# Kernel tuning notes

Measured on AMD Instinct MI355X. Metric: run time of the kernel, lower is better.

The kernel has to match this reference:

```python
import jax, jax.numpy as jnp
import numpy as np

B, S, H, D, R = 2, 2048, 16, 128, 16
HID = H * D
ROPE_BASE = 10000.0


def _rotate_half(x):
    x1, x2 = x[..., : D // 2], x[..., D // 2:]
    return jnp.concatenate((-x2, x1), axis=-1)


def _sin_cos(position_ids):
    # full-dim RoPE (rope_fraction == 1)
    inv_freq = 1.0 / (ROPE_BASE ** (jnp.arange(0, D, 2, dtype=jnp.float32) / D))  # [D/2]
    freqs = position_ids.astype(jnp.float32)[..., None] * inv_freq  # [B,S,D/2]
    emb = jnp.concatenate((freqs, freqs), axis=-1)  # [B,S,D]
    # add head axis -> [B,1,S,D]
    return jnp.sin(emb)[:, None], jnp.cos(emb)[:, None]


def setup_inputs() -> dict:
    key = jax.random.key(0)
    ks = jax.random.split(key, 6)
    q = jax.random.normal(ks[0], (B, S, HID), dtype=jnp.float32)
    k = jax.random.normal(ks[1], (B, S, HID), dtype=jnp.float32)
    v = jax.random.normal(ks[2], (B, S, HID), dtype=jnp.float32)
    position_ids = jnp.tile(jnp.arange(S, dtype=jnp.int64)[None], (B, 1))
    causal = jnp.tril(jnp.ones((S, S), dtype=bool))
    attention_mask = jnp.where(causal, 0.0, -1e9).astype(jnp.float32)
    attention_mask = jnp.broadcast_to(attention_mask[None, None], (B, 1, S, S))
    k_registers = jax.random.normal(ks[3], (1, H, R, D), dtype=jnp.float32)
    v_registers = jax.random.normal(ks[4], (1, H, R, D), dtype=jnp.float32)
    return {
        "query_states": q,
        "key_states": k,
        "value_states": v,
        "position_ids": position_ids,
        "attention_mask": attention_mask,
        "k_registers": k_registers,
        "v_registers": v_registers,
    }


def reference(query_states, key_states, value_states, position_ids,
              attention_mask, k_registers, v_registers):
    bsz, q_len, _ = query_states.shape
    # [B,S,H*D] -> [B,H,S,D]
    q = query_states.reshape(bsz, q_len, H, D).transpose(0, 2, 1, 3)
    k = key_states.reshape(bsz, -1, H, D).transpose(0, 2, 1, 3)
    v = value_states.reshape(bsz, -1, H, D).transpose(0, 2, 1, 3)

    sin, cos = _sin_cos(position_ids)
    q = q * cos + _rotate_half(q) * sin
    k = k * cos + _rotate_half(k) * sin

    # concat learned register K/V tokens along kv-length
    k = jnp.concatenate((k, jnp.broadcast_to(k_registers, (bsz, H, R, D))), axis=2)
    v = jnp.concatenate((v, jnp.broadcast_to(v_registers, (bsz, H, R, D))), axis=2)
    mask = jnp.concatenate(
        (attention_mask,
         jnp.zeros(attention_mask.shape[:-1] + (R,), dtype=attention_mask.dtype)),
        axis=-1)

    scale = 1.0 / np.sqrt(D).astype(np.float32)
    scores = jnp.einsum('bhqd,bhkd->bhqk', q, k * scale) + mask  # [B,H,S,S+R]
    probs = jax.nn.softmax(scores.astype(jnp.float32), axis=-1).astype(q.dtype)
    out = jnp.einsum('bhqk,bhkd->bhqd', probs, v)
    return out.transpose(0, 2, 1, 3).reshape(bsz, q_len, H * D)
```

## Files before the change

### kernel.cpp

```cpp
#include <hip/hip_runtime.h>

#define S_LEN 2048
#define HID   2048
#define NH    16
#define HD    128
#define NREG  16
#define KPAD  2112
#define NBH   32

typedef float f32x4 __attribute__((ext_vector_type(4)));
typedef short s16x8 __attribute__((ext_vector_type(8)));

#define ROPE_C  0.20762050593046014f
#define INV2PI  0.15915494309189535f
#define TWOPI   6.283185307179586f
#define QSCALE  0.08838834764831845f

__device__ __forceinline__ unsigned short f2bf(float f) {
    union { float f; unsigned int u; } x; x.f = f;
    return (unsigned short)((x.u + 0x7FFFu + ((x.u >> 16) & 1u)) >> 16);
}
__device__ __forceinline__ unsigned short f2bf_t(float f) {
    union { float f; unsigned int u; } x; x.f = f;
    return (unsigned short)(x.u >> 16);
}
__device__ __forceinline__ void gl_lds16(const unsigned short* g, unsigned short* l) {
    __builtin_amdgcn_global_load_lds((const __attribute__((address_space(1))) void*)g,
                                     (__attribute__((address_space(3))) void*)l, 16, 0, 0);
}

__global__ void prep_kernel(const float* __restrict__ k, const float* __restrict__ v,
                            const int* __restrict__ pos,
                            const float* __restrict__ kreg, const float* __restrict__ vreg,
                            unsigned short* __restrict__ Kb, unsigned short* __restrict__ Vt) {
    int kt = blockIdx.x % 33;
    int bh = blockIdx.x / 33;
    int b = bh >> 4, h = bh & 15;
    int tid = threadIdx.x;

    {
        int dh = tid & 63, wv = tid >> 6;
        if (kt < 32) {
            float inv = exp2f((float)dh * -ROPE_C);
            #pragma unroll 4
            for (int j = 0; j < 16; ++j) {
                int key = wv * 16 + j;
                int s = kt * 64 + key;
                float p = (float)pos[b * S_LEN + s];
                float rev = p * inv * INV2PI;
                rev -= rintf(rev);
                float a2 = rev * TWOPI;
                float sn = __sinf(a2), cs = __cosf(a2);
                const float* kp = k + (size_t)(b * S_LEN + s) * HID + h * HD + dh;
                float k1 = kp[0], k2 = kp[64];
                size_t ko = (size_t)(bh * KPAD + s) * HD + dh;
                Kb[ko]      = f2bf(k1 * cs - k2 * sn);
                Kb[ko + 64] = f2bf(k2 * cs + k1 * sn);
            }
        } else {
            #pragma unroll 4
            for (int j = 0; j < 16; ++j) {
                int r = wv * 16 + j;
                float k1 = 0.f, k2 = 0.f;
                if (r < NREG) {
                    const float* kp = kreg + (h * NREG + r) * HD + dh;
                    k1 = kp[0]; k2 = kp[64];
                }
                size_t ko = (size_t)(bh * KPAD + 2048 + r) * HD + dh;
                Kb[ko]      = f2bf(k1);
                Kb[ko + 64] = f2bf(k2);
            }
        }
    }

    __shared__ unsigned short T[64][136];
    {
        int key = tid >> 2, c = tid & 3;
        #pragma unroll
        for (int i = 0; i < 4; ++i) {
            int d0 = c * 32 + i * 8;
            float vals[8];
            if (kt < 32) {
                const float* src = v + (size_t)(b * S_LEN + kt * 64 + key) * HID + h * HD + d0;
                float4 a = *(const float4*)src, bb = *(const float4*)(src + 4);
                vals[0]=a.x; vals[1]=a.y; vals[2]=a.z; vals[3]=a.w;
                vals[4]=bb.x; vals[5]=bb.y; vals[6]=bb.z; vals[7]=bb.w;
            } else if (key < NREG) {
                const float* src = vreg + (h * NREG + key) * HD + d0;
                float4 a = *(const float4*)src, bb = *(const float4*)(src + 4);
                vals[0]=a.x; vals[1]=a.y; vals[2]=a.z; vals[3]=a.w;
                vals[4]=bb.x; vals[5]=bb.y; vals[6]=bb.z; vals[7]=bb.w;
            } else {
                #pragma unroll
                for (int n = 0; n < 8; ++n) vals[n] = 0.f;
            }
            unsigned short tmp[8];
            #pragma unroll
            for (int n = 0; n < 8; ++n) tmp[n] = f2bf(vals[n]);
            *(uint4*)(&T[key][d0]) = *(const uint4*)tmp;
        }
    }
    __syncthreads();
    {
        int d = tid >> 1, half = tid & 1;
        unsigned short buf[32];
        #pragma unroll
        for (int i = 0; i < 32; ++i) buf[i] = T[half * 32 + i][d];
        uint4* dst = (uint4*)(Vt + ((size_t)(bh * HD + d)) * KPAD + kt * 64 + half * 32);
        const uint4* bp = (const uint4*)buf;
        #pragma unroll
        for (int i = 0; i < 4; ++i) dst[i] = bp[i];
    }
}

__global__ __launch_bounds__(256, 2)
void attn_kernel(const float* __restrict__ q, const int* __restrict__ pos,
                 const unsigned short* __restrict__ Kb, const unsigned short* __restrict__ Vt,
                 float* __restrict__ out) {
    __shared__ unsigned short Klds[64 * 128];
    __shared__ unsigned short Vtl[128 * 64];
    __shared__ unsigned short Plds[4 * 32 * 72];

    int idx = blockIdx.x;
    int bh  = idx & 31;
    int j5  = idx >> 5;
    int t   = (idx < 256) ? (15 - 2 * j5) : (2 * (j5 - 8));
    int b = bh >> 4, h = bh & 15;
    int tid = threadIdx.x, w = tid >> 6, lane = tid & 63;
    int quad = lane >> 4, k15 = lane & 15;
    int s0q = t * 128;

    const unsigned short* kg[4]; unsigned short* klp[4];
    const unsigned short* vg[4]; unsigned short* vlp[4];
    {
        int krow = 16 * w + (lane >> 4);
        #pragma unroll
        for (int j = 0; j < 4; ++j) {
            int key = krow + 4 * j;
            kg[j]  = Kb + ((size_t)bh * KPAD + key) * HD + (((lane & 15) ^ (key & 15)) << 3);
            klp[j] = Klds + (16 * w + 4 * j) * HD;
        }
        int drow = 32 * w + (lane >> 3);
        int vsw  = ((lane & 7) ^ (lane >> 3)) << 3;
        #pragma unroll
        for (int j = 0; j < 4; ++j) {
            vg[j]  = Vt + ((size_t)bh * HD + drow + 8 * j) * KPAD + vsw;
            vlp[j] = Vtl + (32 * w + 8 * j) * 64;
        }
    }

    s16x8 qa[2][4];
    #pragma unroll
    for (int mt = 0; mt < 2; ++mt) {
        int s = s0q + w * 32 + mt * 16 + k15;
        float pp = (float)pos[b * S_LEN + s];
        const float* qrow = q + (size_t)(b * S_LEN + s) * HID + h * HD + quad * 8;
        float lo[2][8], hi[2][8];
        #pragma unroll
        for (int kc = 0; kc < 2; ++kc) {
            float4 a  = *(const float4*)(qrow + kc * 32);
            float4 c  = *(const float4*)(qrow + kc * 32 + 4);
            lo[kc][0]=a.x; lo[kc][1]=a.y; lo[kc][2]=a.z; lo[kc][3]=a.w;
            lo[kc][4]=c.x; lo[kc][5]=c.y; lo[kc][6]=c.z; lo[kc][7]=c.w;
            float4 a2 = *(const float4*)(qrow + kc * 32 + 64);
            float4 c2 = *(const float4*)(qrow + kc * 32 + 68);
            hi[kc][0]=a2.x; hi[kc][1]=a2.y; hi[kc][2]=a2.z; hi[kc][3]=a2.w;
            hi[kc][4]=c2.x; hi[kc][5]=c2.y; hi[kc][6]=c2.z; hi[kc][7]=c2.w;
        }
        #pragma unroll
        for (int kc = 0; kc < 2; ++kc)
            #pragma unroll
            for (int j = 0; j < 8; ++j) {
                int dh = kc * 32 + quad * 8 + j;
                float inv = exp2f((float)dh * -ROPE_C);
                float rev = pp * inv * INV2PI;
                rev -= rintf(rev);
                float a2r = rev * TWOPI;
                float sn = __sinf(a2r), cs = __cosf(a2r);
                float qlo = lo[kc][j], qhi = hi[kc][j];
                qa[mt][kc][j]     = (short)f2bf((qlo * cs - qhi * sn) * QSCALE);
                qa[mt][kc + 2][j] = (short)f2bf((qhi * cs + qlo * sn) * QSCALE);
            }
    }

    f32x4 oacc[2][8];
    float lsum[2][4];
    #pragma unroll
    for (int mt = 0; mt < 2; ++mt) {
        #pragma unroll
        for (int nc = 0; nc < 8; ++nc) oacc[mt][nc] = (f32x4){0.f, 0.f, 0.f, 0.f};
        #pragma unroll
        for (int r = 0; r < 4; ++r) lsum[mt][r] = 0.f;
    }

    auto stage = [&](int kbase) {
        size_t ko = (size_t)kbase * HD;
        #pragma unroll
        for (int j = 0; j < 4; ++j) gl_lds16(kg[j] + ko, klp[j]);
        #pragma unroll
        for (int j = 0; j < 4; ++j) gl_lds16(vg[j] + kbase, vlp[j]);
    };

    auto tile = [&](int coff, int mode) {
        f32x4 sc[2][4];
        #pragma unroll
        for (int mt = 0; mt < 2; ++mt)
            #pragma unroll
            for (int nc = 0; nc < 4; ++nc) sc[mt][nc] = (f32x4){0.f, 0.f, 0.f, 0.f};
        #pragma unroll
        for (int kc = 0; kc < 4; ++kc)
            #pragma unroll
            for (int nc = 0; nc < 4; ++nc) {
                if (mode == 2 && nc > 0) continue;
                const s16x8 bf = *(const s16x8*)(Klds + (nc * 16 + k15) * HD +
                                                 (((4 * kc + quad) ^ k15) << 3));
                #pragma unroll
                for (int mt = 0; mt < 2; ++mt)
                    sc[mt][nc] = __builtin_amdgcn_mfma_f32_16x16x32_bf16(qa[mt][kc], bf, sc[mt][nc], 0, 0, 0);
            }
        #pragma unroll
        for (int mt = 0; mt < 2; ++mt) {
            int rowb = w * 32 + mt * 16 + quad * 4;
            #pragma unroll
            for (int r = 0; r < 4; ++r) {
                float p[4];
                #pragma unroll
                for (int nc = 0; nc < 4; ++nc) {
                    if (mode == 2 && nc > 0) { p[nc] = 0.f; continue; }
                    float e = __expf(sc[mt][nc][r]);
                    bool valid = (mode == 1) ? (coff + nc * 16 + k15 <= rowb + r)
                               : (mode == 2) ? (k15 < NREG) : true;
                    p[nc] = valid ? e : 0.f;
                }
                lsum[mt][r] += (p[0] + p[1]) + (p[2] + p[3]);
                int prow = w * (32 * 72) + (mt * 16 + quad * 4 + r) * 72 + k15;
                Plds[prow]      = f2bf_t(p[0]);
                Plds[prow + 16] = f2bf_t(p[1]);
                Plds[prow + 32] = f2bf_t(p[2]);
                Plds[prow + 48] = f2bf_t(p[3]);
            }
        }
        #pragma unroll
        for (int kc = 0; kc < 2; ++kc) {
            if (mode == 2 && kc > 0) break;
            s16x8 pf[2];
            #pragma unroll
            for (int mt = 0; mt < 2; ++mt)
                pf[mt] = *(const s16x8*)(Plds + w * (32 * 72) + (mt * 16 + k15) * 72 +
                                         kc * 32 + quad * 8);
            #pragma unroll
            for (int nc = 0; nc < 8; ++nc) {
                const s16x8 vf = *(const s16x8*)(Vtl + (nc * 16 + k15) * 64 +
                                                 (((4 * kc + quad) ^ (k15 & 7)) << 3));
                #pragma unroll
                for (int mt = 0; mt < 2; ++mt)
                    oacc[mt][nc] = __builtin_amdgcn_mfma_f32_16x16x32_bf16(pf[mt], vf, oacc[mt][nc], 0, 0, 0);
            }
        }
    };

    int nfull = 2 * t;
    for (int kt = 0; kt < nfull; ++kt) {
        __syncthreads();
        stage(kt * 64);
        __syncthreads();
        tile(0, 0);
    }
    #pragma unroll
    for (int dt = 0; dt < 2; ++dt) {
        __syncthreads();
        stage((2 * t + dt) * 64);
        __syncthreads();
        tile(64 * dt, 1);
    }
    __syncthreads();
    stage(2048);
    __syncthreads();
    tile(0, 2);

    #pragma unroll
    for (int mt = 0; mt < 2; ++mt)
        #pragma unroll
        for (int r = 0; r < 4; ++r) {
            float lv = lsum[mt][r];
            #pragma unroll
            for (int off = 1; off < 16; off <<= 1) lv += __shfl_xor(lv, off);
            float invl = 1.0f / lv;
            size_t row = (size_t)(b * S_LEN + s0q + w * 32 + mt * 16 + quad * 4 + r) * HID
                         + h * HD + k15;
            #pragma unroll
            for (int nc = 0; nc < 8; ++nc)
                out[row + nc * 16] = oacc[mt][nc][r] * invl;
        }
}

extern "C" void kernel_launch(void* const* d_in, const int* in_sizes, int n_in,
                              void* d_out, int out_size, void* d_ws, size_t ws_size,
                              hipStream_t stream) {
    const float* q    = (const float*)d_in[0];
    const float* k    = (const float*)d_in[1];
    const float* v    = (const float*)d_in[2];
    const int*   pos  = (const int*)d_in[3];
    const float* kreg = (const float*)d_in[5];
    const float* vreg = (const float*)d_in[6];
    float* out = (float*)d_out;

    unsigned short* Kb = (unsigned short*)d_ws;
    unsigned short* Vt = Kb + (size_t)NBH * KPAD * HD;

    prep_kernel<<<dim3(NBH * 33), dim3(256), 0, stream>>>(k, v, pos, kreg, vreg, Kb, Vt);
    attn_kernel<<<dim3(512), dim3(256), 0, stream>>>(q, pos, Kb, Vt, out);
}
```

Baseline: 226.9 us.

## Use 8 waves per block with double-buffered K staging

The attention kernel now runs 512 threads per block, so each wave owns 16 query rows instead of 32, which cuts per-wave register use (one m-tile instead of two). K tiles are double-buffered in LDS and the next K tile is prefetched while the current one is processed. V is still single-buffered and is staged alongside the K prefetch. The main loop is restructured with a barrier between score and PV phases. The trade-off is a higher wave count per block and the LDS cost of a second K buffer, with less MFMA reuse of each K/V fragment per wave.

```diff
diff --git a/kernel.cpp b/kernel.cpp
--- a/kernel.cpp
+++ b/kernel.cpp
@@ -113,13 +113,13 @@
     }
 }
 
-__global__ __launch_bounds__(256, 2)
+__global__ __launch_bounds__(512, 4)
 void attn_kernel(const float* __restrict__ q, const int* __restrict__ pos,
                  const unsigned short* __restrict__ Kb, const unsigned short* __restrict__ Vt,
                  float* __restrict__ out) {
-    __shared__ unsigned short Klds[64 * 128];
+    __shared__ unsigned short Klds[2][64 * 128];
     __shared__ unsigned short Vtl[128 * 64];
-    __shared__ unsigned short Plds[4 * 32 * 72];
+    __shared__ unsigned short Plds[8 * 16 * 72];
 
     int idx = blockIdx.x;
     int bh  = idx & 31;
@@ -130,29 +130,37 @@
     int quad = lane >> 4, k15 = lane & 15;
     int s0q = t * 128;
 
-    const unsigned short* kg[4]; unsigned short* klp[4];
-    const unsigned short* vg[4]; unsigned short* vlp[4];
-    {
-        int krow = 16 * w + (lane >> 4);
-        #pragma unroll
-        for (int j = 0; j < 4; ++j) {
-            int key = krow + 4 * j;
-            kg[j]  = Kb + ((size_t)bh * KPAD + key) * HD + (((lane & 15) ^ (key & 15)) << 3);
-            klp[j] = Klds + (16 * w + 4 * j) * HD;
-        }
-        int drow = 32 * w + (lane >> 3);
-        int vsw  = ((lane & 7) ^ (lane >> 3)) << 3;
-        #pragma unroll
-        for (int j = 0; j < 4; ++j) {
-            vg[j]  = Vt + ((size_t)bh * HD + drow + 8 * j) * KPAD + vsw;
-            vlp[j] = Vtl + (32 * w + 8 * j) * 64;
-        }
-    }
-
-    s16x8 qa[2][4];
-    #pragma unroll
-    for (int mt = 0; mt < 2; ++mt) {
-        int s = s0q + w * 32 + mt * 16 + k15;
+    const unsigned short* Kb_bh = Kb + (size_t)bh * KPAD * HD;
+    const unsigned short* Vt_bh = Vt + (size_t)bh * HD * KPAD;
+    int koff[2], klo[2], voff[2], vlo[2];
+    #pragma unroll
+    for (int j = 0; j < 2; ++j) {
+        int row = 4 * (w + 8 * j) + (lane >> 4);
+        int gd  = (lane & 15) ^ (row & 15);
+        koff[j] = row * HD + (gd << 3);
+        klo[j]  = 4 * (w + 8 * j) * HD;
+        int d   = 8 * (w + 8 * j) + (lane >> 3);
+        int gk  = (lane & 7) ^ (d & 7);
+        voff[j] = d * KPAD + (gk << 3);
+        vlo[j]  = 8 * (w + 8 * j) * 64;
+    }
+
+    auto stageK = [&](int kbase, int buf) {
+        #pragma unroll
+        for (int j = 0; j < 2; ++j)
+            gl_lds16(Kb_bh + (size_t)kbase * HD + koff[j], &Klds[buf][klo[j]]);
+    };
+    auto stageV = [&](int kbase) {
+        #pragma unroll
+        for (int j = 0; j < 2; ++j)
+            gl_lds16(Vt_bh + kbase + voff[j], Vtl + vlo[j]);
+    };
+
+    stageK(0, 0);
+
+    s16x8 qa[4];
+    {
+        int s = s0q + w * 16 + k15;
         float pp = (float)pos[b * S_LEN + s];
         const float* qrow = q + (size_t)(b * S_LEN + s) * HID + h * HD + quad * 8;
         float lo[2][8], hi[2][8];
@@ -178,120 +186,89 @@
                 float a2r = rev * TWOPI;
                 float sn = __sinf(a2r), cs = __cosf(a2r);
                 float qlo = lo[kc][j], qhi = hi[kc][j];
-                qa[mt][kc][j]     = (short)f2bf((qlo * cs - qhi * sn) * QSCALE);
-                qa[mt][kc + 2][j] = (short)f2bf((qhi * cs + qlo * sn) * QSCALE);
-            }
-    }
-
-    f32x4 oacc[2][8];
-    float lsum[2][4];
-    #pragma unroll
-    for (int mt = 0; mt < 2; ++mt) {
-        #pragma unroll
-        for (int nc = 0; nc < 8; ++nc) oacc[mt][nc] = (f32x4){0.f, 0.f, 0.f, 0.f};
-        #pragma unroll
-        for (int r = 0; r < 4; ++r) lsum[mt][r] = 0.f;
-    }
-
-    auto stage = [&](int kbase) {
-        size_t ko = (size_t)kbase * HD;
-        #pragma unroll
-        for (int j = 0; j < 4; ++j) gl_lds16(kg[j] + ko, klp[j]);
-        #pragma unroll
-        for (int j = 0; j < 4; ++j) gl_lds16(vg[j] + kbase, vlp[j]);
-    };
-
-    auto tile = [&](int coff, int mode) {
-        f32x4 sc[2][4];
-        #pragma unroll
-        for (int mt = 0; mt < 2; ++mt)
-            #pragma unroll
-            for (int nc = 0; nc < 4; ++nc) sc[mt][nc] = (f32x4){0.f, 0.f, 0.f, 0.f};
+                qa[kc][j]     = (short)f2bf((qlo * cs - qhi * sn) * QSCALE);
+                qa[kc + 2][j] = (short)f2bf((qhi * cs + qlo * sn) * QSCALE);
+            }
+    }
+
+    f32x4 oacc[8];
+    float lsum[4];
+    #pragma unroll
+    for (int nc = 0; nc < 8; ++nc) oacc[nc] = (f32x4){0.f, 0.f, 0.f, 0.f};
+    #pragma unroll
+    for (int r = 0; r < 4; ++r) lsum[r] = 0.f;
+
+    unsigned short* pwave = Plds + w * (16 * 72);
+
+    int nt = 2 * t + 3;
+    for (int kt = 0; kt < nt; ++kt) {
+        int mode = (kt < 2 * t) ? 0 : (kt < 2 * t + 2) ? 1 : 2;
+        int coff = 64 * (kt - 2 * t);
+
+        __syncthreads();
+        stageV((kt < 2 * t + 2) ? kt * 64 : 2048);
+        if (kt + 1 < nt)
+            stageK((kt + 1 < 2 * t + 2) ? (kt + 1) * 64 : 2048, (kt + 1) & 1);
+
+        const unsigned short* kb = Klds[kt & 1];
+        f32x4 sc[4];
+        #pragma unroll
+        for (int nc = 0; nc < 4; ++nc) sc[nc] = (f32x4){0.f, 0.f, 0.f, 0.f};
         #pragma unroll
         for (int kc = 0; kc < 4; ++kc)
             #pragma unroll
             for (int nc = 0; nc < 4; ++nc) {
                 if (mode == 2 && nc > 0) continue;
-                const s16x8 bf = *(const s16x8*)(Klds + (nc * 16 + k15) * HD +
+                const s16x8 bf = *(const s16x8*)(kb + (nc * 16 + k15) * HD +
                                                  (((4 * kc + quad) ^ k15) << 3));
-                #pragma unroll
-                for (int mt = 0; mt < 2; ++mt)
-                    sc[mt][nc] = __builtin_amdgcn_mfma_f32_16x16x32_bf16(qa[mt][kc], bf, sc[mt][nc], 0, 0, 0);
-            }
-        #pragma unroll
-        for (int mt = 0; mt < 2; ++mt) {
-            int rowb = w * 32 + mt * 16 + quad * 4;
-            #pragma unroll
-            for (int r = 0; r < 4; ++r) {
-                float p[4];
-                #pragma unroll
-                for (int nc = 0; nc < 4; ++nc) {
-                    if (mode == 2 && nc > 0) { p[nc] = 0.f; continue; }
-                    float e = __expf(sc[mt][nc][r]);
-                    bool valid = (mode == 1) ? (coff + nc * 16 + k15 <= rowb + r)
-                               : (mode == 2) ? (k15 < NREG) : true;
-                    p[nc] = valid ? e : 0.f;
-                }
-                lsum[mt][r] += (p[0] + p[1]) + (p[2] + p[3]);
-                int prow = w * (32 * 72) + (mt * 16 + quad * 4 + r) * 72 + k15;
-                Plds[prow]      = f2bf_t(p[0]);
-                Plds[prow + 16] = f2bf_t(p[1]);
-                Plds[prow + 32] = f2bf_t(p[2]);
-                Plds[prow + 48] = f2bf_t(p[3]);
-            }
-        }
+                sc[nc] = __builtin_amdgcn_mfma_f32_16x16x32_bf16(qa[kc], bf, sc[nc], 0, 0, 0);
+            }
+
+        int rowb = w * 16 + quad * 4;
+        #pragma unroll
+        for (int r = 0; r < 4; ++r) {
+            float p[4];
+            #pragma unroll
+            for (int nc = 0; nc < 4; ++nc) {
+                if (mode == 2 && nc > 0) { p[nc] = 0.f; continue; }
+                float e = __expf(sc[nc][r]);
+                bool valid = (mode == 1) ? (coff + nc * 16 + k15 <= rowb + r) : true;
+                p[nc] = valid ? e : 0.f;
+            }
+            lsum[r] += (p[0] + p[1]) + (p[2] + p[3]);
+            int prow = (quad * 4 + r) * 72 + k15;
+            pwave[prow]      = f2bf_t(p[0]);
+            pwave[prow + 16] = f2bf_t(p[1]);
+            pwave[prow + 32] = f2bf_t(p[2]);
+            pwave[prow + 48] = f2bf_t(p[3]);
+        }
+
+        __syncthreads();
+
         #pragma unroll
         for (int kc = 0; kc < 2; ++kc) {
             if (mode == 2 && kc > 0) break;
-            s16x8 pf[2];
-            #pragma unroll
-            for (int mt = 0; mt < 2; ++mt)
-                pf[mt] = *(const s16x8*)(Plds + w * (32 * 72) + (mt * 16 + k15) * 72 +
-                                         kc * 32 + quad * 8);
+            const s16x8 pf = *(const s16x8*)(pwave + k15 * 72 + kc * 32 + quad * 8);
             #pragma unroll
             for (int nc = 0; nc < 8; ++nc) {
                 const s16x8 vf = *(const s16x8*)(Vtl + (nc * 16 + k15) * 64 +
                                                  (((4 * kc + quad) ^ (k15 & 7)) << 3));
-                #pragma unroll
-                for (int mt = 0; mt < 2; ++mt)
-                    oacc[mt][nc] = __builtin_amdgcn_mfma_f32_16x16x32_bf16(pf[mt], vf, oacc[mt][nc], 0, 0, 0);
-            }
-        }
-    };
-
-    int nfull = 2 * t;
-    for (int kt = 0; kt < nfull; ++kt) {
-        __syncthreads();
-        stage(kt * 64);
-        __syncthreads();
-        tile(0, 0);
-    }
-    #pragma unroll
-    for (int dt = 0; dt < 2; ++dt) {
-        __syncthreads();
-        stage((2 * t + dt) * 64);
-        __syncthreads();
-        tile(64 * dt, 1);
-    }
-    __syncthreads();
-    stage(2048);
-    __syncthreads();
-    tile(0, 2);
-
-    #pragma unroll
-    for (int mt = 0; mt < 2; ++mt)
-        #pragma unroll
-        for (int r = 0; r < 4; ++r) {
-            float lv = lsum[mt][r];
-            #pragma unroll
-            for (int off = 1; off < 16; off <<= 1) lv += __shfl_xor(lv, off);
-            float invl = 1.0f / lv;
-            size_t row = (size_t)(b * S_LEN + s0q + w * 32 + mt * 16 + quad * 4 + r) * HID
-                         + h * HD + k15;
-            #pragma unroll
-            for (int nc = 0; nc < 8; ++nc)
-                out[row + nc * 16] = oacc[mt][nc][r] * invl;
-        }
+                oacc[nc] = __builtin_amdgcn_mfma_f32_16x16x32_bf16(pf, vf, oacc[nc], 0, 0, 0);
+            }
+        }
+    }
+
+    #pragma unroll
+    for (int r = 0; r < 4; ++r) {
+        float lv = lsum[r];
+        #pragma unroll
+        for (int off = 1; off < 16; off <<= 1) lv += __shfl_xor(lv, off);
+        float invl = 1.0f / lv;
+        size_t row = (size_t)(b * S_LEN + s0q + w * 16 + quad * 4 + r) * HID + h * HD + k15;
+        #pragma unroll
+        for (int nc = 0; nc < 8; ++nc)
+            out[row + nc * 16] = oacc[nc][r] * invl;
+    }
 }
 
 extern "C" void kernel_launch(void* const* d_in, const int* in_sizes, int n_in,
@@ -309,5 +286,5 @@
     unsigned short* Vt = Kb + (size_t)NBH * KPAD * HD;
 
     prep_kernel<<<dim3(NBH * 33), dim3(256), 0, stream>>>(k, v, pos, kreg, vreg, Kb, Vt);
-    attn_kernel<<<dim3(512), dim3(256), 0, stream>>>(q, pos, Kb, Vt, out);
-}
+    attn_kernel<<<dim3(512), dim3(512), 0, stream>>>(q, pos, Kb, Vt, out);
+}
```

After: 233.3 us. +2.8%, slower.
